# Kernel tuning notes

Measured on AMD Instinct MI355X. Metric: run time of the kernel, lower is better.

## Reference

```python
import jax, jax.numpy as jnp
import numpy as np

K = 16                      # instance ids 1..K (0 = background, ignored)
DELTA_V, DELTA_D, GAMMA = 0.5, 1.5, 0.001
W_CLUST, W_CENTER, W_BOUND, W_LOVASZ = 0.1, 0.1, 0.05, 0.01


def _pdist(x, y):
    # x: [..., n, d], y: [..., m, d] -> euclidean distances [..., n, m]
    x2 = (x * x).sum(-1)[..., :, None]
    y2 = (y * y).sum(-1)[..., None, :]
    d2 = x2 + y2 - 2.0 * jnp.einsum('...nd,...md->...nm', x, y)
    return jnp.sqrt(jnp.maximum(d2, 0.0))


def _losses(points, embeddings, labels):
    # F.normalize(embeddings, p=2, dim=2)
    emb = embeddings / jnp.maximum(
        jnp.linalg.norm(embeddings, axis=-1, keepdims=True), 1e-12)
    B, N, D = emb.shape
    ids = jnp.arange(1, K + 1)
    M = (labels[..., None] == ids).astype(emb.dtype)            # [B,N,K]
    cnt = M.sum(1)                                               # [B,K] (>=1 by construction)
    # raw per-instance feature centers (mean of normalized embeddings)
    fc = jnp.einsum('bnk,bnd->bkd', M, emb) / cnt[..., None]     # [B,K,D]
    cen = fc / jnp.maximum(jnp.linalg.norm(fc, axis=-1, keepdims=True), 1e-12)

    # ---- clustering: variance term ----
    d_nc = _pdist(emb, cen)                                      # [B,N,K]
    var_loss = ((jnp.maximum(d_nc - DELTA_V, 0.0) * M).sum(1) / cnt).sum() / (B + 1e-6)

    # ---- clustering: inter-center distance term ----
    cd = _pdist(cen, cen)                                        # [B,K,K]
    off = 1.0 - jnp.eye(K, dtype=emb.dtype)
    dist_loss = ((jnp.maximum(2.0 * DELTA_D - cd, 0.0) * off).sum((1, 2))
                 / (K * (K - 1))).sum() / (B + 1e-6)

    # ---- clustering: regularizer (Frobenius norm of centers) ----
    reg_loss = jnp.linalg.norm(cen.reshape(B, -1), axis=1).sum() * GAMMA / (B + 1e-6)

    # ---- center loss: spatial dist * feature dist to per-instance means ----
    gc = jnp.einsum('bnk,bnc->bkc', M, points) / cnt[..., None]  # geometric centers [B,K,3]
    sd = _pdist(points, gc)                                      # [B,N,K]
    fd = _pdist(emb, fc)                                         # [B,N,K] (fc NOT renormalized)
    center_loss = ((sd * fd * M).sum(1) / cnt).sum() / B

    # ---- boundary loss: full NxN cdist, zero same-instance entries ----
    dm = _pdist(emb, emb)                                        # [B,N,N]
    same = labels[:, :, None] == labels[:, None, :]
    bd = dm * (~same).astype(emb.dtype)
    boundary_loss = jnp.maximum(DELTA_D - bd, 0.0).mean(axis=(1, 2)).sum() / B

    enorm = jnp.maximum(jnp.linalg.norm(emb, axis=-1), 1e-8)     # [B,N]
    mnorm = jnp.maximum(jnp.linalg.norm(fc, axis=-1), 1e-8)      # [B,K]
    sim = jnp.einsum('bnd,bkd->bnk', emb, fc) / (enorm[..., None] * mnorm[:, None, :])
    order = jnp.argsort(-sim, axis=1)                            # descending sort per (b,k)
    ss = jnp.take_along_axis(sim, order, axis=1)                 # sorted similarities
    sm = jnp.take_along_axis(M, order, axis=1)                   # masks in sorted order
    inter = cnt[:, None, :] - jnp.cumsum(sm, axis=1)
    union = cnt[:, None, :] + jnp.cumsum(1.0 - sm, axis=1)
    jac = 1.0 - inter / union
    jd = jnp.concatenate([jac[:, :1], jac[:, 1:] - jac[:, :-1]], axis=1)
    lovasz_loss = (jnp.maximum(ss, 0.0) * jd).sum() / B

    total = (W_CLUST * (var_loss + dist_loss + reg_loss)
             + W_CENTER * center_loss + W_BOUND * boundary_loss
             + W_LOVASZ * lovasz_loss)
    return jnp.stack([total, var_loss, dist_loss, reg_loss,
                      center_loss, boundary_loss, lovasz_loss])


def setup_inputs() -> dict:
    key = jax.random.key(0)
    k1, k2, k3 = jax.random.split(key, 3)
    B, N, D = 4, 4096, 64
    points = jax.random.normal(k1, (B, N, 3), jnp.float32)
    embeddings = jax.random.normal(k2, (B, N, D), jnp.float32)
    labels = jax.random.randint(k3, (B, N), 0, K + 1)
    # guarantee every id 0..K appears in each cloud (matches torch unique() set)
    labels = labels.at[:, :K + 1].set(jnp.arange(K + 1))
    return {"points": points, "embeddings": embeddings, "instance_labels": labels}


def reference(points, embeddings, instance_labels):
    # returns stacked [total, var, dist, reg, center, boundary, lovasz]
    return _losses(points, embeddings, instance_labels)
```

## Files before the change

kernel.cpp:

```cpp
#include <hip/hip_runtime.h>

#define BB 4
#define NN 4096
#define DD 64
#define KK 16
#define NBUCK 2048
#define NCHB 144
#define NBND (NCHB * BB)
#define NLOV 64

#define OFF_EMB   0u
#define OFF_NRM2  1048576u
#define OFF_PFC   1064960u
#define OFF_PGC   1327104u
#define OFF_PCNT  1339392u
#define OFF_FC    1343488u
#define OFF_CEN   1347584u
#define OFF_GC    1351680u
#define OFF_FCN   1351872u
#define OFF_FCN2  1351936u
#define OFF_CEN2  1352000u
#define OFF_GC2   1352064u
#define OFF_CNTF  1352128u
#define OFF_BND   1352192u
#define OFF_VAR   1352768u
#define OFF_CENL  1352832u
#define OFF_LOV   1352896u
#define OFF_PH    1353216u
#define OFF_EMBH  1615360u

typedef __attribute__((ext_vector_type(8))) short bf16x8;
typedef __attribute__((ext_vector_type(4))) float f32x4;

#define FSQRT(x) __builtin_amdgcn_sqrtf(x)
#define FRCP(x)  __builtin_amdgcn_rcpf(x)
#define FRSQ(x)  __builtin_amdgcn_rsqf(x)

__device__ __forceinline__ ushort f2bf(float x){
  unsigned u = __float_as_uint(x);
  return (ushort)((u + 0x7FFFu + ((u >> 16) & 1u)) >> 16);
}

__device__ __forceinline__ float blockReduceSum(float v, float* sbuf){
  int t = threadIdx.x;
  #pragma unroll
  for (int off = 32; off > 0; off >>= 1) v += __shfl_xor(v, off, 64);
  if ((t & 63) == 0) sbuf[t >> 6] = v;
  __syncthreads();
  float s = 0.f;
  if (t == 0){
    int nw = blockDim.x >> 6;
    for (int i = 0; i < nw; i++) s += sbuf[i];
  }
  __syncthreads();
  return s;
}

__device__ __forceinline__ double blockReduceD(double v, double* sbuf){
  int t = threadIdx.x;
  #pragma unroll
  for (int off = 32; off > 0; off >>= 1) v += __shfl_xor(v, off, 64);
  if ((t & 63) == 0) sbuf[t >> 6] = v;
  __syncthreads();
  double s = 0.0;
  if (t == 0){
    for (int i = 0; i < 4; i++) s += sbuf[i];
  }
  __syncthreads();
  return s;
}

__global__ void knormacc(const float* __restrict__ emb, const float* __restrict__ pts,
                         const int* __restrict__ lbl, float* __restrict__ ws){
  __shared__ float fcl[KK * DD];
  __shared__ float gcl[KK * 3];
  __shared__ float cntl[KK];
  int t = threadIdx.x;
  for (int i = t; i < KK * DD; i += 256) fcl[i] = 0.f;
  if (t < KK * 3) gcl[t] = 0.f;
  if (t < KK) cntl[t] = 0.f;
  __syncthreads();

  int lane = t & 63, w = t >> 6;
  int b = blockIdx.x >> 6;
  int local = blockIdx.x & 63;
  int base = local * 64 + w * 16;
  const float* E = emb + (size_t)b * NN * DD;
  float* EN = ws + OFF_EMB + (size_t)b * NN * DD;
  ushort* EH = (ushort*)(ws + OFF_EMBH) + (size_t)b * NN * DD;

  for (int i = 0; i < 16; i++){
    int n = base + i;
    float v = E[(size_t)n * DD + lane];
    float ss = v * v;
    #pragma unroll
    for (int off = 1; off < 64; off <<= 1) ss += __shfl_xor(ss, off, 64);
    float nrm = FSQRT(ss);
    float scale = FRCP(fmaxf(nrm, 1e-12f));
    float vn = v * scale;
    EN[(size_t)n * DD + lane] = vn;
    EH[(size_t)n * DD + lane] = f2bf(vn);
    if (lane == 0) ws[OFF_NRM2 + b * NN + n] = ss * scale * scale;
    int l = lbl[b * NN + n];
    if (l >= 1 && l <= KK){
      int k = l - 1;
      atomicAdd(&fcl[k * DD + lane], vn);
      if (lane < 3) atomicAdd(&gcl[k * 3 + lane], pts[((size_t)b * NN + n) * 3 + lane]);
      if (lane == 0) atomicAdd(&cntl[k], 1.0f);
    }
  }
  __syncthreads();
  for (int i = t; i < KK * DD; i += 256)
    ws[OFF_PFC + (size_t)blockIdx.x * KK * DD + i] = fcl[i];
  if (t < KK * 3) ws[OFF_PGC + blockIdx.x * KK * 3 + t] = gcl[t];
  if (t < KK)     ws[OFF_PCNT + blockIdx.x * KK + t] = cntl[t];
}

__global__ void kcenters(float* __restrict__ ws){
  __shared__ float accL[4][DD];
  int bk = blockIdx.x;
  int b = bk >> 4, k = bk & 15;
  int t = threadIdx.x;
  int lane = t & 63, w = t >> 6;
  float s = 0.f;
  #pragma unroll
  for (int j = 0; j < 16; j++)
    s += ws[OFF_PFC + (size_t)((b * 64 + w * 16 + j) * KK + k) * DD + lane];
  accL[w][lane] = s;
  __syncthreads();
  for (int i = t; i < 4096; i += 256) ws[OFF_PH + bk * 4096 + i] = 0.f;
  if (w == 0){
    float fsum = accL[0][lane] + accL[1][lane] + accL[2][lane] + accL[3][lane];
    float cp  = ws[OFF_PCNT + (b * 64 + lane) * KK + k];
    float gp0 = ws[OFF_PGC + ((b * 64 + lane) * KK + k) * 3 + 0];
    float gp1 = ws[OFF_PGC + ((b * 64 + lane) * KK + k) * 3 + 1];
    float gp2 = ws[OFF_PGC + ((b * 64 + lane) * KK + k) * 3 + 2];
    #pragma unroll
    for (int off = 1; off < 64; off <<= 1){
      cp  += __shfl_xor(cp, off, 64);
      gp0 += __shfl_xor(gp0, off, 64);
      gp1 += __shfl_xor(gp1, off, 64);
      gp2 += __shfl_xor(gp2, off, 64);
    }
    float inv_c = FRCP(cp);
    float f = fsum * inv_c;
    ws[OFF_FC + (size_t)(b * KK + k) * DD + lane] = f;
    float n2 = f * f;
    #pragma unroll
    for (int off = 1; off < 64; off <<= 1) n2 += __shfl_xor(n2, off, 64);
    float fn = FSQRT(n2);
    float inv = FRCP(fmaxf(fn, 1e-12f));
    float ce = f * inv;
    ws[OFF_CEN + (size_t)(b * KK + k) * DD + lane] = ce;
    float g0 = gp0 * inv_c, g1 = gp1 * inv_c, g2 = gp2 * inv_c;
    if (lane == 0){
      ws[OFF_GC + (b * KK + k) * 3 + 0] = g0;
      ws[OFF_GC + (b * KK + k) * 3 + 1] = g1;
      ws[OFF_GC + (b * KK + k) * 3 + 2] = g2;
      ws[OFF_FCN  + b * KK + k] = fn;
      ws[OFF_FCN2 + b * KK + k] = n2;
      ws[OFF_CEN2 + b * KK + k] = n2 * inv * inv;
      ws[OFF_GC2  + b * KK + k] = g0 * g0 + g1 * g1 + g2 * g2;
      ws[OFF_CNTF + b * KK + k] = cp;
    }
  }
}

__global__ __launch_bounds__(256, 4) void kfused(const int* __restrict__ lbl,
                                                 const ushort* __restrict__ EHg,
                                                 const float* __restrict__ pts,
                                                 float* __restrict__ ws){
  __shared__ float red[16];
  int t = threadIdx.x;

  if (blockIdx.x < NLOV){
    __shared__ float invmfnS[KK], invfcS[KK], invCS[KK], fcn2S[KK], cen2S[KK], gc2S[KK];
    __shared__ float gcS[KK][3];
    int g = blockIdx.x * 256 + t;
    int b = g >> 12;
    int n = g & (NN - 1);
    if (t < KK){
      float fcn = ws[OFF_FCN + b * KK + t];
      invmfnS[t] = FRCP(fmaxf(fcn, 1e-8f));
      invfcS[t]  = FRCP(fmaxf(fcn, 1e-12f));
      invCS[t]   = FRCP(ws[OFF_CNTF + b * KK + t]);
      fcn2S[t]   = ws[OFF_FCN2 + b * KK + t];
      cen2S[t]   = ws[OFF_CEN2 + b * KK + t];
      gc2S[t]    = ws[OFF_GC2  + b * KK + t];
      gcS[t][0]  = ws[OFF_GC + (b * KK + t) * 3 + 0];
      gcS[t][1]  = ws[OFF_GC + (b * KK + t) * 3 + 1];
      gcS[t][2]  = ws[OFF_GC + (b * KK + t) * 3 + 2];
    }
    __syncthreads();

    const float* EN = ws + OFF_EMB + (size_t)(b * NN + n) * DD;
    float4 e4[16];
    #pragma unroll
    for (int i = 0; i < 16; i++) e4[i] = *(const float4*)&EN[i * 4];
    float nrm2 = ws[OFF_NRM2 + b * NN + n];
    float rs = FRSQ(nrm2);
    int l = lbl[b * NN + n];
    float p0 = pts[((size_t)b * NN + n) * 3 + 0];
    float p1 = pts[((size_t)b * NN + n) * 3 + 1];
    float p2 = pts[((size_t)b * NN + n) * 3 + 2];
    float p2sum = p0 * p0 + p1 * p1 + p2 * p2;
    float varA = 0.f, cenA = 0.f;

    for (int k = 0; k < KK; k++){
      const float* FCk = ws + OFF_FC + (size_t)(b * KK + k) * DD;
      float dx = 0.f, dy = 0.f, dz = 0.f, dw = 0.f;
      #pragma unroll
      for (int i = 0; i < 16; i++){
        float4 f = *(const float4*)&FCk[i * 4];
        dx += e4[i].x * f.x; dy += e4[i].y * f.y;
        dz += e4[i].z * f.z; dw += e4[i].w * f.w;
      }
      float dot = (dx + dy) + (dz + dw);
      float sim = dot * rs * invmfnS[k];
      int m = (l == k + 1) ? 1 : 0;
      if (sim > 0.f){
        int q = (int)(sim * (float)NBUCK);
        q = q > NBUCK - 1 ? NBUCK - 1 : q;
        int qi = NBUCK - 1 - q;
        unsigned* H = (unsigned*)(ws + OFF_PH) + (size_t)(b * KK + k) * 4096;
        float* S = ws + OFF_PH + (size_t)(b * KK + k) * 4096 + 2048;
        atomicAdd(&H[qi], 1u + ((unsigned)m << 16));
        atomicAdd(&S[qi], sim);
      }
      if (m){
        float dotc = dot * invfcS[k];
        float dnc = FSQRT(fmaxf(nrm2 + cen2S[k] - 2.f * dotc, 0.f));
        varA += fmaxf(dnc - 0.5f, 0.f) * invCS[k];
        float fd = FSQRT(fmaxf(nrm2 + fcn2S[k] - 2.f * dot, 0.f));
        float sd2 = p2sum + gc2S[k] - 2.f * (p0 * gcS[k][0] + p1 * gcS[k][1] + p2 * gcS[k][2]);
        cenA += FSQRT(fmaxf(sd2, 0.f)) * fd * invCS[k];
      }
    }
    float vs = blockReduceSum(varA, red);
    if (t == 0) ws[OFF_VAR + blockIdx.x] = vs;
    float cs = blockReduceSum(cenA, red);
    if (t == 0) ws[OFF_CENL + blockIdx.x] = cs;
  } else {
    int q = blockIdx.x - NLOV;
    int b = q / NCHB;
    int cq = q - b * NCHB;
    int ti = 0, rem = cq;
    while (rem >= ((32 - ti + 3) >> 2)){ rem -= (32 - ti + 3) >> 2; ti++; }
    int tj0 = ti + rem * 4;
    int nt = 32 - tj0; if (nt > 4) nt = 4;

    int lane = t & 63, w = t >> 6;
    int lm = lane & 15;
    int rif = (lane >> 4) * 4;
    int lk = (lane >> 4) * 8;
    const ushort* E = EHg + (size_t)b * NN * DD;
    const float* NR = ws + OFF_NRM2 + b * NN;
    const int* LB = lbl + b * NN;

    bf16x8 a[2][2];
    #pragma unroll
    for (int rb = 0; rb < 2; rb++)
      #pragma unroll
      for (int kh = 0; kh < 2; kh++)
        a[rb][kh] = *(const bf16x8*)&E[(size_t)(ti * 128 + w * 32 + rb * 16 + lm) * DD + kh * 32 + lk];

    float nAr[8]; int lAr[8];
    #pragma unroll
    for (int rb = 0; rb < 2; rb++)
      #pragma unroll
      for (int r = 0; r < 4; r++){
        int gi = ti * 128 + w * 32 + rb * 16 + rif + r;
        nAr[rb * 4 + r] = NR[gi];
        lAr[rb * 4 + r] = LB[gi];
      }

    float sum = 0.f;
    for (int tt = 0; tt < nt; tt++){
      int tj = tj0 + tt;
      bool diag = (tj == ti);
      #pragma unroll
      for (int pass = 0; pass < 2; pass++){
        float nBr[4]; int lBr[4];
        #pragma unroll
        for (int cb = 0; cb < 4; cb++){
          int gj = tj * 128 + (pass * 4 + cb) * 16 + lm;
          nBr[cb] = NR[gj];
          lBr[cb] = LB[gj];
        }
        f32x4 ac[2][4];
        #pragma unroll
        for (int rb = 0; rb < 2; rb++)
          #pragma unroll
          for (int cb = 0; cb < 4; cb++) ac[rb][cb] = (f32x4){0.f, 0.f, 0.f, 0.f};
        #pragma unroll
        for (int cb = 0; cb < 4; cb++){
          #pragma unroll
          for (int kh = 0; kh < 2; kh++){
            bf16x8 bb = *(const bf16x8*)&E[(size_t)(tj * 128 + (pass * 4 + cb) * 16 + lm) * DD + kh * 32 + lk];
            ac[0][cb] = __builtin_amdgcn_mfma_f32_16x16x32_bf16(a[0][kh], bb, ac[0][cb], 0, 0, 0);
            ac[1][cb] = __builtin_amdgcn_mfma_f32_16x16x32_bf16(a[1][kh], bb, ac[1][cb], 0, 0, 0);
          }
        }
        if (diag){
          #pragma unroll
          for (int rb = 0; rb < 2; rb++)
            #pragma unroll
            for (int cb = 0; cb < 4; cb++)
              #pragma unroll
              for (int r = 0; r < 4; r++){
                float d2 = fmaxf(nAr[rb * 4 + r] + nBr[cb] - 2.f * ac[rb][cb][r], 0.f);
                if (lAr[rb * 4 + r] == lBr[cb]) d2 = 0.f;
                float f = fmaxf(1.5f - FSQRT(d2), 0.f);
                int gi = w * 32 + rb * 16 + rif + r;
                int gj = (pass * 4 + cb) * 16 + lm;
                sum += (gi < gj) ? f : 0.f;
              }
        } else {
          #pragma unroll
          for (int rb = 0; rb < 2; rb++)
            #pragma unroll
            for (int cb = 0; cb < 4; cb++)
              #pragma unroll
              for (int r = 0; r < 4; r++){
                float d2 = fmaxf(nAr[rb * 4 + r] + nBr[cb] - 2.f * ac[rb][cb][r], 0.f);
                if (lAr[rb * 4 + r] == lBr[cb]) d2 = 0.f;
                sum += fmaxf(1.5f - FSQRT(d2), 0.f);
              }
        }
      }
    }
    float s = blockReduceSum(sum, red);
    if (t == 0) ws[OFF_BND + q] = s;
  }
}

__global__ void klov2(float* __restrict__ ws){
  __shared__ unsigned wsum[4];
  __shared__ float red[16];
  int bk = blockIdx.x;
  int b = bk >> 4, k = bk & 15;
  int t = threadIdx.x;
  int lane = t & 63, w = t >> 6;
  const unsigned* H = (const unsigned*)(ws + OFF_PH) + (size_t)bk * 4096;
  const float* S = ws + OFF_PH + (size_t)bk * 4096 + 2048;
  float C = ws[OFF_CNTF + b * KK + k];

  int base = t * 8;
  unsigned hv[8]; float sv[8];
  #pragma unroll
  for (int i = 0; i < 8; i++){ hv[i] = H[base + i]; sv[i] = S[base + i]; }
  unsigned loc[8];
  unsigned run = 0;
  #pragma unroll
  for (int i = 0; i < 8; i++){ loc[i] = run; run += hv[i]; }
  unsigned tot = run, sc = tot;
  #pragma unroll
  for (int off = 1; off < 64; off <<= 1){
    unsigned v = __shfl_up(sc, off, 64);
    if (lane >= off) sc += v;
  }
  if (lane == 63) wsum[w] = sc;
  __syncthreads();
  unsigned wbase = 0;
  #pragma unroll
  for (int w2 = 0; w2 < 4; w2++) if (w2 < w) wbase += wsum[w2];
  unsigned ex = wbase + sc - tot;

  float contrib = 0.f;
  #pragma unroll
  for (int i = 0; i < 8; i++){
    unsigned h = hv[i];
    unsigned g = h & 0xFFFFu, mu = h >> 16;
    if (g){
      unsigned pre = ex + loc[i];
      float i0 = (float)(pre & 0xFFFFu), c0 = (float)(pre >> 16);
      float i1 = i0 + (float)g, c1 = c0 + (float)mu;
      float jac0 = 1.f - (C - c0) * FRCP(C + i0 - c0);
      float jac1 = 1.f - (C - c1) * FRCP(C + i1 - c1);
      contrib += sv[i] * (jac1 - jac0) * FRCP((float)g);
    }
  }
  float ls = blockReduceSum(contrib, red);
  if (t == 0) ws[OFF_LOV + bk] = ls;
}

__global__ void kfinal(const float* __restrict__ ws, float* __restrict__ out){
  __shared__ double dred[4];
  __shared__ float red[16];
  int t = threadIdx.x;
  double bs = 0.0;
  for (int i = t; i < NBND; i += 256) bs += (double)ws[OFF_BND + i];
  bs = blockReduceD(bs, dred);
  double lv = (t < 64) ? (double)ws[OFF_LOV + t] : 0.0;
  lv = blockReduceD(lv, dred);
  double va = (t < 64) ? (double)ws[OFF_VAR + t] : 0.0;
  va = blockReduceD(va, dred);
  double ce = (t < 64) ? (double)ws[OFF_CENL + t] : 0.0;
  ce = blockReduceD(ce, dred);

  double di = 0.0, rg = 0.0;
  int i = t >> 4, j = t & 15;
  for (int b = 0; b < BB; b++){
    float v = 0.f;
    if (i != j){
      float dot = 0.f;
      #pragma unroll
      for (int d = 0; d < DD; d++)
        dot += ws[OFF_CEN + (size_t)(b * KK + i) * DD + d] * ws[OFF_CEN + (size_t)(b * KK + j) * DD + d];
      float cd = FSQRT(fmaxf(ws[OFF_CEN2 + b * KK + i] + ws[OFF_CEN2 + b * KK + j] - 2.f * dot, 0.f));
      v = fmaxf(3.f - cd, 0.f);
    }
    float s = blockReduceSum(v, red);
    if (t == 0){
      di += (double)(s / 240.f);
      float s2 = 0.f;
      for (int k = 0; k < KK; k++) s2 += ws[OFF_CEN2 + b * KK + k];
      rg += (double)(FSQRT(s2) * 0.001f);
    }
  }
  if (t == 0){
    double var_l  = va / (4.0 + 1e-6);
    double dist_l = di / (4.0 + 1e-6);
    double reg_l  = rg / (4.0 + 1e-6);
    double cen_l  = ce / 4.0;
    double bnd_l  = (2.0 * bs + 1.5 * (double)NN * BB) / ((double)NN * NN * BB);
    double lov_l  = lv / 4.0;
    double total = 0.1 * (var_l + dist_l + reg_l) + 0.1 * cen_l + 0.05 * bnd_l + 0.01 * lov_l;
    out[0] = (float)total; out[1] = (float)var_l; out[2] = (float)dist_l;
    out[3] = (float)reg_l; out[4] = (float)cen_l; out[5] = (float)bnd_l;
    out[6] = (float)lov_l;
  }
}

extern "C" void kernel_launch(void* const* d_in, const int* in_sizes, int n_in,
                              void* d_out, int out_size, void* d_ws, size_t ws_size,
                              hipStream_t stream){
  const float* pts = (const float*)d_in[0];
  const float* emb = (const float*)d_in[1];
  const int* lbl   = (const int*)d_in[2];
  float* out = (float*)d_out;
  float* ws = (float*)d_ws;

  hipLaunchKernelGGL(knormacc, dim3(256), dim3(256), 0, stream, emb, pts, lbl, ws);
  hipLaunchKernelGGL(kcenters, dim3(64),  dim3(256), 0, stream, ws);
  hipLaunchKernelGGL(kfused,   dim3(NLOV + NBND), dim3(256), 0, stream,
                     lbl, (const ushort*)(ws + OFF_EMBH), pts, ws);
  hipLaunchKernelGGL(klov2,    dim3(64),  dim3(256), 0, stream, ws);
  hipLaunchKernelGGL(kfinal,   dim3(1),   dim3(256), 0, stream, ws, out);
}
```

Before: 77.77 us.

## Merge five kernel launches into one cooperative persistent kernel with grid syncs

The five-kernel pipeline becomes a single cooperative kernel with a 256-block grid. Its phases (normalize/accumulate, centers, lovasz+boundary, lovasz scan, final) are separated by grid.sync(), and the old kernels remain as a fallback if the cooperative launch fails. The aim is to remove per-launch overhead and inter-kernel gaps. The tradeoffs are grid-wide barrier cost, running the 640 fused work units on only 256 blocks (several rounds instead of one wave), and possibly higher register pressure, since the fused kernel is the union of all phases under launch bounds.

```diff
diff --git a/kernel.cpp b/kernel.cpp
--- a/kernel.cpp
+++ b/kernel.cpp
@@ -1,4 +1,5 @@
 #include <hip/hip_runtime.h>
+#include <hip/hip_cooperative_groups.h>
 
 #define BB 4
 #define NN 4096
@@ -8,6 +9,8 @@
 #define NCHB 144
 #define NBND (NCHB * BB)
 #define NLOV 64
+#define NUNIT (NLOV + NBND)
+#define CGRID 256
 
 #define OFF_EMB   0u
 #define OFF_NRM2  1048576u
@@ -70,20 +73,20 @@
   return s;
 }
 
-__global__ void knormacc(const float* __restrict__ emb, const float* __restrict__ pts,
-                         const int* __restrict__ lbl, float* __restrict__ ws){
-  __shared__ float fcl[KK * DD];
-  __shared__ float gcl[KK * 3];
-  __shared__ float cntl[KK];
+
+__device__ void phase_norm(int blk, const float* __restrict__ emb,
+                           const float* __restrict__ pts, const int* __restrict__ lbl,
+                           float* __restrict__ ws,
+                           float* fcl, float* gclS, float* cntl){
   int t = threadIdx.x;
   for (int i = t; i < KK * DD; i += 256) fcl[i] = 0.f;
-  if (t < KK * 3) gcl[t] = 0.f;
+  if (t < KK * 3) gclS[t] = 0.f;
   if (t < KK) cntl[t] = 0.f;
   __syncthreads();
 
   int lane = t & 63, w = t >> 6;
-  int b = blockIdx.x >> 6;
-  int local = blockIdx.x & 63;
+  int b = blk >> 6;
+  int local = blk & 63;
   int base = local * 64 + w * 16;
   const float* E = emb + (size_t)b * NN * DD;
   float* EN = ws + OFF_EMB + (size_t)b * NN * DD;
@@ -105,20 +108,18 @@
     if (l >= 1 && l <= KK){
       int k = l - 1;
       atomicAdd(&fcl[k * DD + lane], vn);
-      if (lane < 3) atomicAdd(&gcl[k * 3 + lane], pts[((size_t)b * NN + n) * 3 + lane]);
+      if (lane < 3) atomicAdd(&gclS[k * 3 + lane], pts[((size_t)b * NN + n) * 3 + lane]);
       if (lane == 0) atomicAdd(&cntl[k], 1.0f);
     }
   }
   __syncthreads();
   for (int i = t; i < KK * DD; i += 256)
-    ws[OFF_PFC + (size_t)blockIdx.x * KK * DD + i] = fcl[i];
-  if (t < KK * 3) ws[OFF_PGC + blockIdx.x * KK * 3 + t] = gcl[t];
-  if (t < KK)     ws[OFF_PCNT + blockIdx.x * KK + t] = cntl[t];
-}
-
-__global__ void kcenters(float* __restrict__ ws){
-  __shared__ float accL[4][DD];
-  int bk = blockIdx.x;
+    ws[OFF_PFC + (size_t)blk * KK * DD + i] = fcl[i];
+  if (t < KK * 3) ws[OFF_PGC + blk * KK * 3 + t] = gclS[t];
+  if (t < KK)     ws[OFF_PCNT + blk * KK + t] = cntl[t];
+}
+
+__device__ void phase_centers(int bk, float* __restrict__ ws, float (*accL)[DD]){
   int b = bk >> 4, k = bk & 15;
   int t = threadIdx.x;
   int lane = t & 63, w = t >> 6;
@@ -166,178 +167,173 @@
   }
 }
 
-__global__ __launch_bounds__(256, 4) void kfused(const int* __restrict__ lbl,
-                                                 const ushort* __restrict__ EHg,
-                                                 const float* __restrict__ pts,
-                                                 float* __restrict__ ws){
-  __shared__ float red[16];
-  int t = threadIdx.x;
-
-  if (blockIdx.x < NLOV){
-    __shared__ float invmfnS[KK], invfcS[KK], invCS[KK], fcn2S[KK], cen2S[KK], gc2S[KK];
-    __shared__ float gcS[KK][3];
-    int g = blockIdx.x * 256 + t;
-    int b = g >> 12;
-    int n = g & (NN - 1);
-    if (t < KK){
-      float fcn = ws[OFF_FCN + b * KK + t];
-      invmfnS[t] = FRCP(fmaxf(fcn, 1e-8f));
-      invfcS[t]  = FRCP(fmaxf(fcn, 1e-12f));
-      invCS[t]   = FRCP(ws[OFF_CNTF + b * KK + t]);
-      fcn2S[t]   = ws[OFF_FCN2 + b * KK + t];
-      cen2S[t]   = ws[OFF_CEN2 + b * KK + t];
-      gc2S[t]    = ws[OFF_GC2  + b * KK + t];
-      gcS[t][0]  = ws[OFF_GC + (b * KK + t) * 3 + 0];
-      gcS[t][1]  = ws[OFF_GC + (b * KK + t) * 3 + 1];
-      gcS[t][2]  = ws[OFF_GC + (b * KK + t) * 3 + 2];
-    }
-    __syncthreads();
-
-    const float* EN = ws + OFF_EMB + (size_t)(b * NN + n) * DD;
-    float4 e4[16];
-    #pragma unroll
-    for (int i = 0; i < 16; i++) e4[i] = *(const float4*)&EN[i * 4];
-    float nrm2 = ws[OFF_NRM2 + b * NN + n];
-    float rs = FRSQ(nrm2);
-    int l = lbl[b * NN + n];
-    float p0 = pts[((size_t)b * NN + n) * 3 + 0];
-    float p1 = pts[((size_t)b * NN + n) * 3 + 1];
-    float p2 = pts[((size_t)b * NN + n) * 3 + 2];
-    float p2sum = p0 * p0 + p1 * p1 + p2 * p2;
-    float varA = 0.f, cenA = 0.f;
-
-    for (int k = 0; k < KK; k++){
-      const float* FCk = ws + OFF_FC + (size_t)(b * KK + k) * DD;
-      float dx = 0.f, dy = 0.f, dz = 0.f, dw = 0.f;
+__device__ void phase_lovasz1(int blk, const int* __restrict__ lbl,
+                              const float* __restrict__ pts, float* __restrict__ ws,
+                              float* red, float* invmfnS, float* invfcS, float* invCS,
+                              float* fcn2S, float* cen2S, float* gc2S, float (*gcS)[3]){
+  int t = threadIdx.x;
+  int g = blk * 256 + t;
+  int b = g >> 12;
+  int n = g & (NN - 1);
+  if (t < KK){
+    float fcn = ws[OFF_FCN + b * KK + t];
+    invmfnS[t] = FRCP(fmaxf(fcn, 1e-8f));
+    invfcS[t]  = FRCP(fmaxf(fcn, 1e-12f));
+    invCS[t]   = FRCP(ws[OFF_CNTF + b * KK + t]);
+    fcn2S[t]   = ws[OFF_FCN2 + b * KK + t];
+    cen2S[t]   = ws[OFF_CEN2 + b * KK + t];
+    gc2S[t]    = ws[OFF_GC2  + b * KK + t];
+    gcS[t][0]  = ws[OFF_GC + (b * KK + t) * 3 + 0];
+    gcS[t][1]  = ws[OFF_GC + (b * KK + t) * 3 + 1];
+    gcS[t][2]  = ws[OFF_GC + (b * KK + t) * 3 + 2];
+  }
+  __syncthreads();
+
+  const float* EN = ws + OFF_EMB + (size_t)(b * NN + n) * DD;
+  float4 e4[16];
+  #pragma unroll
+  for (int i = 0; i < 16; i++) e4[i] = *(const float4*)&EN[i * 4];
+  float nrm2 = ws[OFF_NRM2 + b * NN + n];
+  float rs = FRSQ(nrm2);
+  int l = lbl[b * NN + n];
+  float p0 = pts[((size_t)b * NN + n) * 3 + 0];
+  float p1 = pts[((size_t)b * NN + n) * 3 + 1];
+  float p2 = pts[((size_t)b * NN + n) * 3 + 2];
+  float p2sum = p0 * p0 + p1 * p1 + p2 * p2;
+  float varA = 0.f, cenA = 0.f;
+
+  for (int k = 0; k < KK; k++){
+    const float* FCk = ws + OFF_FC + (size_t)(b * KK + k) * DD;
+    float dx = 0.f, dy = 0.f, dz = 0.f, dw = 0.f;
+    #pragma unroll
+    for (int i = 0; i < 16; i++){
+      float4 f = *(const float4*)&FCk[i * 4];
+      dx += e4[i].x * f.x; dy += e4[i].y * f.y;
+      dz += e4[i].z * f.z; dw += e4[i].w * f.w;
+    }
+    float dot = (dx + dy) + (dz + dw);
+    float sim = dot * rs * invmfnS[k];
+    int m = (l == k + 1) ? 1 : 0;
+    if (sim > 0.f){
+      int q = (int)(sim * (float)NBUCK);
+      q = q > NBUCK - 1 ? NBUCK - 1 : q;
+      int qi = NBUCK - 1 - q;
+      unsigned* H = (unsigned*)(ws + OFF_PH) + (size_t)(b * KK + k) * 4096;
+      float* S = ws + OFF_PH + (size_t)(b * KK + k) * 4096 + 2048;
+      atomicAdd(&H[qi], 1u + ((unsigned)m << 16));
+      atomicAdd(&S[qi], sim);
+    }
+    if (m){
+      float dotc = dot * invfcS[k];
+      float dnc = FSQRT(fmaxf(nrm2 + cen2S[k] - 2.f * dotc, 0.f));
+      varA += fmaxf(dnc - 0.5f, 0.f) * invCS[k];
+      float fd = FSQRT(fmaxf(nrm2 + fcn2S[k] - 2.f * dot, 0.f));
+      float sd2 = p2sum + gc2S[k] - 2.f * (p0 * gcS[k][0] + p1 * gcS[k][1] + p2 * gcS[k][2]);
+      cenA += FSQRT(fmaxf(sd2, 0.f)) * fd * invCS[k];
+    }
+  }
+  float vs = blockReduceSum(varA, red);
+  if (t == 0) ws[OFF_VAR + blk] = vs;
+  float cs = blockReduceSum(cenA, red);
+  if (t == 0) ws[OFF_CENL + blk] = cs;
+}
+
+__device__ void phase_boundary(int q, const int* __restrict__ lbl,
+                               const ushort* __restrict__ EHg,
+                               float* __restrict__ ws, float* red){
+  int t = threadIdx.x;
+  int b = q / NCHB;
+  int cq = q - b * NCHB;
+  int ti = 0, rem = cq;
+  while (rem >= ((32 - ti + 3) >> 2)){ rem -= (32 - ti + 3) >> 2; ti++; }
+  int tj0 = ti + rem * 4;
+  int nt = 32 - tj0; if (nt > 4) nt = 4;
+
+  int lane = t & 63, w = t >> 6;
+  int lm = lane & 15;
+  int rif = (lane >> 4) * 4;
+  int lk = (lane >> 4) * 8;
+  const ushort* E = EHg + (size_t)b * NN * DD;
+  const float* NR = ws + OFF_NRM2 + b * NN;
+  const int* LB = lbl + b * NN;
+
+  bf16x8 a[2][2];
+  #pragma unroll
+  for (int rb = 0; rb < 2; rb++)
+    #pragma unroll
+    for (int kh = 0; kh < 2; kh++)
+      a[rb][kh] = *(const bf16x8*)&E[(size_t)(ti * 128 + w * 32 + rb * 16 + lm) * DD + kh * 32 + lk];
+
+  float nAr[8]; int lAr[8];
+  #pragma unroll
+  for (int rb = 0; rb < 2; rb++)
+    #pragma unroll
+    for (int r = 0; r < 4; r++){
+      int gi = ti * 128 + w * 32 + rb * 16 + rif + r;
+      nAr[rb * 4 + r] = NR[gi];
+      lAr[rb * 4 + r] = LB[gi];
+    }
+
+  float sum = 0.f;
+  for (int tt = 0; tt < nt; tt++){
+    int tj = tj0 + tt;
+    bool diag = (tj == ti);
+    #pragma unroll
+    for (int pass = 0; pass < 2; pass++){
+      float nBr[4]; int lBr[4];
       #pragma unroll
-      for (int i = 0; i < 16; i++){
-        float4 f = *(const float4*)&FCk[i * 4];
-        dx += e4[i].x * f.x; dy += e4[i].y * f.y;
-        dz += e4[i].z * f.z; dw += e4[i].w * f.w;
+      for (int cb = 0; cb < 4; cb++){
+        int gj = tj * 128 + (pass * 4 + cb) * 16 + lm;
+        nBr[cb] = NR[gj];
+        lBr[cb] = LB[gj];
       }
-      float dot = (dx + dy) + (dz + dw);
-      float sim = dot * rs * invmfnS[k];
-      int m = (l == k + 1) ? 1 : 0;
-      if (sim > 0.f){
-        int q = (int)(sim * (float)NBUCK);
-        q = q > NBUCK - 1 ? NBUCK - 1 : q;
-        int qi = NBUCK - 1 - q;
-        unsigned* H = (unsigned*)(ws + OFF_PH) + (size_t)(b * KK + k) * 4096;
-        float* S = ws + OFF_PH + (size_t)(b * KK + k) * 4096 + 2048;
-        atomicAdd(&H[qi], 1u + ((unsigned)m << 16));
-        atomicAdd(&S[qi], sim);
+      f32x4 ac[2][4];
+      #pragma unroll
+      for (int rb = 0; rb < 2; rb++)
+        #pragma unroll
+        for (int cb = 0; cb < 4; cb++) ac[rb][cb] = (f32x4){0.f, 0.f, 0.f, 0.f};
+      #pragma unroll
+      for (int cb = 0; cb < 4; cb++){
+        #pragma unroll
+        for (int kh = 0; kh < 2; kh++){
+          bf16x8 bb = *(const bf16x8*)&E[(size_t)(tj * 128 + (pass * 4 + cb) * 16 + lm) * DD + kh * 32 + lk];
+          ac[0][cb] = __builtin_amdgcn_mfma_f32_16x16x32_bf16(a[0][kh], bb, ac[0][cb], 0, 0, 0);
+          ac[1][cb] = __builtin_amdgcn_mfma_f32_16x16x32_bf16(a[1][kh], bb, ac[1][cb], 0, 0, 0);
+        }
       }
-      if (m){
-        float dotc = dot * invfcS[k];
-        float dnc = FSQRT(fmaxf(nrm2 + cen2S[k] - 2.f * dotc, 0.f));
-        varA += fmaxf(dnc - 0.5f, 0.f) * invCS[k];
-        float fd = FSQRT(fmaxf(nrm2 + fcn2S[k] - 2.f * dot, 0.f));
-        float sd2 = p2sum + gc2S[k] - 2.f * (p0 * gcS[k][0] + p1 * gcS[k][1] + p2 * gcS[k][2]);
-        cenA += FSQRT(fmaxf(sd2, 0.f)) * fd * invCS[k];
-      }
-    }
-    float vs = blockReduceSum(varA, red);
-    if (t == 0) ws[OFF_VAR + blockIdx.x] = vs;
-    float cs = blockReduceSum(cenA, red);
-    if (t == 0) ws[OFF_CENL + blockIdx.x] = cs;
-  } else {
-    int q = blockIdx.x - NLOV;
-    int b = q / NCHB;
-    int cq = q - b * NCHB;
-    int ti = 0, rem = cq;
-    while (rem >= ((32 - ti + 3) >> 2)){ rem -= (32 - ti + 3) >> 2; ti++; }
-    int tj0 = ti + rem * 4;
-    int nt = 32 - tj0; if (nt > 4) nt = 4;
-
-    int lane = t & 63, w = t >> 6;
-    int lm = lane & 15;
-    int rif = (lane >> 4) * 4;
-    int lk = (lane >> 4) * 8;
-    const ushort* E = EHg + (size_t)b * NN * DD;
-    const float* NR = ws + OFF_NRM2 + b * NN;
-    const int* LB = lbl + b * NN;
-
-    bf16x8 a[2][2];
-    #pragma unroll
-    for (int rb = 0; rb < 2; rb++)
-      #pragma unroll
-      for (int kh = 0; kh < 2; kh++)
-        a[rb][kh] = *(const bf16x8*)&E[(size_t)(ti * 128 + w * 32 + rb * 16 + lm) * DD + kh * 32 + lk];
-
-    float nAr[8]; int lAr[8];
-    #pragma unroll
-    for (int rb = 0; rb < 2; rb++)
-      #pragma unroll
-      for (int r = 0; r < 4; r++){
-        int gi = ti * 128 + w * 32 + rb * 16 + rif + r;
-        nAr[rb * 4 + r] = NR[gi];
-        lAr[rb * 4 + r] = LB[gi];
-      }
-
-    float sum = 0.f;
-    for (int tt = 0; tt < nt; tt++){
-      int tj = tj0 + tt;
-      bool diag = (tj == ti);
-      #pragma unroll
-      for (int pass = 0; pass < 2; pass++){
-        float nBr[4]; int lBr[4];
-        #pragma unroll
-        for (int cb = 0; cb < 4; cb++){
-          int gj = tj * 128 + (pass * 4 + cb) * 16 + lm;
-          nBr[cb] = NR[gj];
-          lBr[cb] = LB[gj];
-        }
-        f32x4 ac[2][4];
+      if (diag){
         #pragma unroll
         for (int rb = 0; rb < 2; rb++)
           #pragma unroll
-          for (int cb = 0; cb < 4; cb++) ac[rb][cb] = (f32x4){0.f, 0.f, 0.f, 0.f};
+          for (int cb = 0; cb < 4; cb++)
+            #pragma unroll
+            for (int r = 0; r < 4; r++){
+              float d2 = fmaxf(nAr[rb * 4 + r] + nBr[cb] - 2.f * ac[rb][cb][r], 0.f);
+              if (lAr[rb * 4 + r] == lBr[cb]) d2 = 0.f;
+              float f = fmaxf(1.5f - FSQRT(d2), 0.f);
+              int gi = w * 32 + rb * 16 + rif + r;
+              int gj = (pass * 4 + cb) * 16 + lm;
+              sum += (gi < gj) ? f : 0.f;
+            }
+      } else {
         #pragma unroll
-        for (int cb = 0; cb < 4; cb++){
+        for (int rb = 0; rb < 2; rb++)
           #pragma unroll
-          for (int kh = 0; kh < 2; kh++){
-            bf16x8 bb = *(const bf16x8*)&E[(size_t)(tj * 128 + (pass * 4 + cb) * 16 + lm) * DD + kh * 32 + lk];
-            ac[0][cb] = __builtin_amdgcn_mfma_f32_16x16x32_bf16(a[0][kh], bb, ac[0][cb], 0, 0, 0);
-            ac[1][cb] = __builtin_amdgcn_mfma_f32_16x16x32_bf16(a[1][kh], bb, ac[1][cb], 0, 0, 0);
-          }
-        }
-        if (diag){
-          #pragma unroll
-          for (int rb = 0; rb < 2; rb++)
+          for (int cb = 0; cb < 4; cb++)
             #pragma unroll
-            for (int cb = 0; cb < 4; cb++)
-              #pragma unroll
-              for (int r = 0; r < 4; r++){
-                float d2 = fmaxf(nAr[rb * 4 + r] + nBr[cb] - 2.f * ac[rb][cb][r], 0.f);
-                if (lAr[rb * 4 + r] == lBr[cb]) d2 = 0.f;
-                float f = fmaxf(1.5f - FSQRT(d2), 0.f);
-                int gi = w * 32 + rb * 16 + rif + r;
-                int gj = (pass * 4 + cb) * 16 + lm;
-                sum += (gi < gj) ? f : 0.f;
-              }
-        } else {
-          #pragma unroll
-          for (int rb = 0; rb < 2; rb++)
-            #pragma unroll
-            for (int cb = 0; cb < 4; cb++)
-              #pragma unroll
-              for (int r = 0; r < 4; r++){
-                float d2 = fmaxf(nAr[rb * 4 + r] + nBr[cb] - 2.f * ac[rb][cb][r], 0.f);
-                if (lAr[rb * 4 + r] == lBr[cb]) d2 = 0.f;
-                sum += fmaxf(1.5f - FSQRT(d2), 0.f);
-              }
-        }
+            for (int r = 0; r < 4; r++){
+              float d2 = fmaxf(nAr[rb * 4 + r] + nBr[cb] - 2.f * ac[rb][cb][r], 0.f);
+              if (lAr[rb * 4 + r] == lBr[cb]) d2 = 0.f;
+              sum += fmaxf(1.5f - FSQRT(d2), 0.f);
+            }
       }
     }
-    float s = blockReduceSum(sum, red);
-    if (t == 0) ws[OFF_BND + q] = s;
-  }
-}
-
-__global__ void klov2(float* __restrict__ ws){
-  __shared__ unsigned wsum[4];
-  __shared__ float red[16];
-  int bk = blockIdx.x;
+  }
+  float s = blockReduceSum(sum, red);
+  if (t == 0) ws[OFF_BND + q] = s;
+}
+
+__device__ void phase_lov2(int bk, float* __restrict__ ws, float* red, unsigned* wsumS){
   int b = bk >> 4, k = bk & 15;
   int t = threadIdx.x;
   int lane = t & 63, w = t >> 6;
@@ -359,11 +355,11 @@
     unsigned v = __shfl_up(sc, off, 64);
     if (lane >= off) sc += v;
   }
-  if (lane == 63) wsum[w] = sc;
+  if (lane == 63) wsumS[w] = sc;
   __syncthreads();
   unsigned wbase = 0;
   #pragma unroll
-  for (int w2 = 0; w2 < 4; w2++) if (w2 < w) wbase += wsum[w2];
+  for (int w2 = 0; w2 < 4; w2++) if (w2 < w) wbase += wsumS[w2];
   unsigned ex = wbase + sc - tot;
 
   float contrib = 0.f;
@@ -384,9 +380,8 @@
   if (t == 0) ws[OFF_LOV + bk] = ls;
 }
 
-__global__ void kfinal(const float* __restrict__ ws, float* __restrict__ out){
-  __shared__ double dred[4];
-  __shared__ float red[16];
+__device__ void phase_final(const float* __restrict__ ws, float* __restrict__ out,
+                            float* red, double* dred){
   int t = threadIdx.x;
   double bs = 0.0;
   for (int i = t; i < NBND; i += 256) bs += (double)ws[OFF_BND + i];
@@ -432,6 +427,87 @@
   }
 }
 
+
+__global__ void knormacc(const float* __restrict__ emb, const float* __restrict__ pts,
+                         const int* __restrict__ lbl, float* __restrict__ ws){
+  __shared__ float fcl[KK * DD];
+  __shared__ float gclS[KK * 3];
+  __shared__ float cntl[KK];
+  phase_norm(blockIdx.x, emb, pts, lbl, ws, fcl, gclS, cntl);
+}
+
+__global__ void kcenters(float* __restrict__ ws){
+  __shared__ float accL[4][DD];
+  phase_centers(blockIdx.x, ws, accL);
+}
+
+__global__ __launch_bounds__(256, 4) void kfused(const int* __restrict__ lbl,
+                                                 const ushort* __restrict__ EHg,
+                                                 const float* __restrict__ pts,
+                                                 float* __restrict__ ws){
+  __shared__ float red[16];
+  if (blockIdx.x < NLOV){
+    __shared__ float invmfnS[KK], invfcS[KK], invCS[KK], fcn2S[KK], cen2S[KK], gc2S[KK];
+    __shared__ float gcS[KK][3];
+    phase_lovasz1(blockIdx.x, lbl, pts, ws, red, invmfnS, invfcS, invCS,
+                  fcn2S, cen2S, gc2S, gcS);
+  } else {
+    phase_boundary(blockIdx.x - NLOV, lbl, EHg, ws, red);
+  }
+}
+
+__global__ void klov2(float* __restrict__ ws){
+  __shared__ unsigned wsumS[4];
+  __shared__ float red[16];
+  phase_lov2(blockIdx.x, ws, red, wsumS);
+}
+
+__global__ void kfinal(const float* __restrict__ ws, float* __restrict__ out){
+  __shared__ double dred[4];
+  __shared__ float red[16];
+  phase_final(ws, out, red, dred);
+}
+
+
+__global__ __launch_bounds__(256, 4) void kall(const float* __restrict__ pts,
+                                               const float* __restrict__ emb,
+                                               const int* __restrict__ lbl,
+                                               float* __restrict__ ws,
+                                               float* __restrict__ out){
+  cooperative_groups::grid_group grid = cooperative_groups::this_grid();
+  __shared__ float fcl[KK * DD];
+  __shared__ float gclS[KK * 3];
+  __shared__ float cntl[KK];
+  __shared__ float accL[4][DD];
+  __shared__ float red[16];
+  __shared__ double dred[4];
+  __shared__ float invmfnS[KK], invfcS[KK], invCS[KK], fcn2S[KK], cen2S[KK], gc2S[KK];
+  __shared__ float gcS[KK][3];
+  __shared__ unsigned wsumS[4];
+
+  phase_norm(blockIdx.x, emb, pts, lbl, ws, fcl, gclS, cntl);
+  grid.sync();
+
+  if (blockIdx.x < 64) phase_centers(blockIdx.x, ws, accL);
+  grid.sync();
+
+  const ushort* EHg = (const ushort*)(ws + OFF_EMBH);
+  for (int unit = blockIdx.x; unit < NUNIT; unit += CGRID){
+    if (unit < NLOV)
+      phase_lovasz1(unit, lbl, pts, ws, red, invmfnS, invfcS, invCS,
+                    fcn2S, cen2S, gc2S, gcS);
+    else
+      phase_boundary(unit - NLOV, lbl, EHg, ws, red);
+    __syncthreads();
+  }
+  grid.sync();
+
+  if (blockIdx.x < 64) phase_lov2(blockIdx.x, ws, red, wsumS);
+  grid.sync();
+
+  if (blockIdx.x == 0) phase_final(ws, out, red, dred);
+}
+
 extern "C" void kernel_launch(void* const* d_in, const int* in_sizes, int n_in,
                               void* d_out, int out_size, void* d_ws, size_t ws_size,
                               hipStream_t stream){
@@ -441,10 +517,16 @@
   float* out = (float*)d_out;
   float* ws = (float*)d_ws;
 
-  hipLaunchKernelGGL(knormacc, dim3(256), dim3(256), 0, stream, emb, pts, lbl, ws);
-  hipLaunchKernelGGL(kcenters, dim3(64),  dim3(256), 0, stream, ws);
-  hipLaunchKernelGGL(kfused,   dim3(NLOV + NBND), dim3(256), 0, stream,
-                     lbl, (const ushort*)(ws + OFF_EMBH), pts, ws);
-  hipLaunchKernelGGL(klov2,    dim3(64),  dim3(256), 0, stream, ws);
-  hipLaunchKernelGGL(kfinal,   dim3(1),   dim3(256), 0, stream, ws, out);
-}
+  void* args[] = { (void*)&pts, (void*)&emb, (void*)&lbl, (void*)&ws, (void*)&out };
+  hipError_t err = hipLaunchCooperativeKernel((const void*)kall, dim3(CGRID), dim3(256),
+                                              args, 0, stream);
+  if (err != hipSuccess){
+    (void)hipGetLastError();
+    hipLaunchKernelGGL(knormacc, dim3(256), dim3(256), 0, stream, emb, pts, lbl, ws);
+    hipLaunchKernelGGL(kcenters, dim3(64),  dim3(256), 0, stream, ws);
+    hipLaunchKernelGGL(kfused,   dim3(NLOV + NBND), dim3(256), 0, stream,
+                       lbl, (const ushort*)(ws + OFF_EMBH), pts, ws);
+    hipLaunchKernelGGL(klov2,    dim3(64),  dim3(256), 0, stream, ws);
+    hipLaunchKernelGGL(kfinal,   dim3(1),   dim3(256), 0, stream, ws, out);
+  }
+}
```

Measured after the change: 218.4 us. +180.8%, slower.
